# Performance work log

Hardware: AMD Instinct MI355X
Metric: run time of the kernel (lower is better)

## Reference

```python
import jax, jax.numpy as jnp
import numpy as np

ORDER = 3        # spline degree k
NUM_KNOTS = 64   # knots param from __init__


def setup_inputs() -> dict:
    key = jax.random.key(0)
    kx, kc = jax.random.split(key)
    # elementwise activation input; values outside [0,1] exercise scipy-style extrapolation
    x = jax.random.normal(kx, (4, 4096, 4096), dtype=jnp.float32)
    # nn.Parameter(torch.randn(num_knots + order))
    coefficients = jax.random.normal(kc, (NUM_KNOTS + ORDER,), dtype=jnp.float32)
    return {"x": x, "coefficients": coefficients}


def reference(x, coefficients):
    p = ORDER
    # knots = np.linspace(0, 1, num_knots + 2*order)
    t = jnp.linspace(0.0, 1.0, NUM_KNOTS + 2 * p).astype(x.dtype)
    n = t.shape[0] - p - 1  # number of basis functions scipy actually uses
    c = coefficients[:n]    # scipy ignores trailing extra coefficients

    # knot-span index; clipping to [p, n-1] reproduces extrapolate=True
    i = jnp.clip(jnp.searchsorted(t, x, side="right") - 1, p, n - 1)

    # de Boor recursion, vectorized over all elements of x
    d = [c[i - p + j] for j in range(p + 1)]  # each has shape of x
    for r in range(1, p + 1):
        for j in range(p, r - 1, -1):
            left = t[i + j - p]
            right = t[i + 1 + j - r]
            alpha = (x - left) / (right - left)
            d[j] = (1.0 - alpha) * d[j - 1] + alpha * d[j]
    return d[p]
```

## Files before the change

### kernel.cpp

```cpp
#include <hip/hip_runtime.h>

#define NCOEF 66
#define H     (1.0f/69.0f)

__device__ __forceinline__ float eval_spline(float xx, const float* __restrict__ c) {
    int i = (int)(xx * 69.0f);
    i = i < 3 ? 3 : (i > 65 ? 65 : i);

    float ti = (float)i * H;
    float u  = xx - ti;
    float u1 = u + H;
    float u2 = u + 2.0f * H;

    float d0 = c[i - 3];
    float d1 = c[i - 2];
    float d2 = c[i - 1];
    float d3 = c[i];

    float a;
    a = u  * 23.0f; d3 = (1.0f - a) * d2 + a * d3;
    a = u1 * 23.0f; d2 = (1.0f - a) * d1 + a * d2;
    a = u2 * 23.0f; d1 = (1.0f - a) * d0 + a * d1;
    a = u  * 34.5f; d3 = (1.0f - a) * d2 + a * d3;
    a = u1 * 34.5f; d2 = (1.0f - a) * d1 + a * d2;
    a = u  * 69.0f; d3 = (1.0f - a) * d2 + a * d3;
    return d3;
}

__global__ __launch_bounds__(256) void spline_kernel(
    const float* __restrict__ x, const float* __restrict__ coef,
    float* __restrict__ out, int n)
{
    __shared__ float c[NCOEF];
    if (threadIdx.x < NCOEF) c[threadIdx.x] = coef[threadIdx.x];
    __syncthreads();

    const int n4     = n >> 2;
    const int stride = gridDim.x * blockDim.x;
    int idx = blockIdx.x * blockDim.x + threadIdx.x;

    for (; idx < n4; idx += stride) {
        float4 xv = reinterpret_cast<const float4*>(x)[idx];
        float4 ov;
        ov.x = eval_spline(xv.x, c);
        ov.y = eval_spline(xv.y, c);
        ov.z = eval_spline(xv.z, c);
        ov.w = eval_spline(xv.w, c);
        reinterpret_cast<float4*>(out)[idx] = ov;
    }

    int tail = (n4 << 2) + (blockIdx.x * blockDim.x + threadIdx.x);
    if (tail < n && (blockIdx.x * blockDim.x + threadIdx.x) < (n & 3)) {
        out[tail] = eval_spline(x[tail], c);
    }
}

extern "C" void kernel_launch(void* const* d_in, const int* in_sizes, int n_in,
                              void* d_out, int out_size, void* d_ws, size_t ws_size,
                              hipStream_t stream) {
    const float* x    = (const float*)d_in[0];
    const float* coef = (const float*)d_in[1];
    float* out        = (float*)d_out;
    int n = in_sizes[0];

    int n4 = n >> 2;
    int threads = 256;
    int blocks = 4096;
    int max_blocks = (n4 + threads - 1) / threads;
    if (blocks > max_blocks) blocks = max_blocks;
    if (blocks < 1) blocks = 1;

    spline_kernel<<<blocks, threads, 0, stream>>>(x, coef, out, n);
}
```

Before: 433.4 us.

## Precompute per-span cubic polynomial coefficients and evaluate via Horner

Each block now converts the 66 B-spline coefficients into per-span cubic polynomial coefficients (uniform-knot B-spline matrix) stored as float4 in shared memory. Per element, the de Boor recursion becomes a single float4 LDS lookup and three FMAs. The grid size also grows to 8192 blocks. The main cost targeted is ALU and LDS work per element; since the kernel streams 256MB in and out it is likely memory bound, so any gain may be small. Rounding differs slightly from the recursion.

```diff
diff --git a/kernel.cpp b/kernel.cpp
--- a/kernel.cpp
+++ b/kernel.cpp
@@ -1,57 +1,56 @@
 #include <hip/hip_runtime.h>
 
 #define NCOEF 66
-#define H     (1.0f/69.0f)
 
-__device__ __forceinline__ float eval_spline(float xx, const float* __restrict__ c) {
-    int i = (int)(xx * 69.0f);
-    i = i < 3 ? 3 : (i > 65 ? 65 : i);
-
-    float ti = (float)i * H;
-    float u  = xx - ti;
-    float u1 = u + H;
-    float u2 = u + 2.0f * H;
-
-    float d0 = c[i - 3];
-    float d1 = c[i - 2];
-    float d2 = c[i - 1];
-    float d3 = c[i];
-
-    float a;
-    a = u  * 23.0f; d3 = (1.0f - a) * d2 + a * d3;
-    a = u1 * 23.0f; d2 = (1.0f - a) * d1 + a * d2;
-    a = u2 * 23.0f; d1 = (1.0f - a) * d0 + a * d1;
-    a = u  * 34.5f; d3 = (1.0f - a) * d2 + a * d3;
-    a = u1 * 34.5f; d2 = (1.0f - a) * d1 + a * d2;
-    a = u  * 69.0f; d3 = (1.0f - a) * d2 + a * d3;
-    return d3;
-}
 
 __global__ __launch_bounds__(256) void spline_kernel(
     const float* __restrict__ x, const float* __restrict__ coef,
     float* __restrict__ out, int n)
 {
-    __shared__ float c[NCOEF];
-    if (threadIdx.x < NCOEF) c[threadIdx.x] = coef[threadIdx.x];
+    __shared__ float  sc[NCOEF];
+    __shared__ float4 tab[NCOEF];
+
+    const int t = threadIdx.x;
+    if (t < NCOEF) sc[t] = coef[t];
+    __syncthreads();
+    if (t >= 3 && t < NCOEF) {
+        float c0 = sc[t - 3], c1 = sc[t - 2], c2 = sc[t - 1], c3 = sc[t];
+        const float k6 = 1.0f / 6.0f;
+        float a0 = (c0 + 4.0f * c1 + c2) * k6;
+        float a1 = (c2 - c0) * 0.5f;
+        float a2 = (c0 - 2.0f * c1 + c2) * 0.5f;
+        float a3 = (c3 - c0 + 3.0f * (c1 - c2)) * k6;
+        tab[t] = make_float4(a0, a1, a2, a3);
+    }
     __syncthreads();
 
     const int n4     = n >> 2;
     const int stride = gridDim.x * blockDim.x;
-    int idx = blockIdx.x * blockDim.x + threadIdx.x;
+    const int gid    = blockIdx.x * blockDim.x + threadIdx.x;
 
-    for (; idx < n4; idx += stride) {
+    for (int idx = gid; idx < n4; idx += stride) {
         float4 xv = reinterpret_cast<const float4*>(x)[idx];
         float4 ov;
-        ov.x = eval_spline(xv.x, c);
-        ov.y = eval_spline(xv.y, c);
-        ov.z = eval_spline(xv.z, c);
-        ov.w = eval_spline(xv.w, c);
+        #pragma unroll
+        for (int e = 0; e < 4; ++e) {
+            float xx = (&xv.x)[e];
+            float xs = xx * 69.0f;
+            int   i  = (int)xs;
+            i = i < 3 ? 3 : (i > 65 ? 65 : i);
+            float s  = xs - (float)i;
+            float4 a = tab[i];
+            (&ov.x)[e] = fmaf(fmaf(fmaf(a.w, s, a.z), s, a.y), s, a.x);
+        }
         reinterpret_cast<float4*>(out)[idx] = ov;
     }
 
-    int tail = (n4 << 2) + (blockIdx.x * blockDim.x + threadIdx.x);
-    if (tail < n && (blockIdx.x * blockDim.x + threadIdx.x) < (n & 3)) {
-        out[tail] = eval_spline(x[tail], c);
+    for (int k = (n4 << 2) + gid; k < n; k += stride) {
+        float xs = x[k] * 69.0f;
+        int   i  = (int)xs;
+        i = i < 3 ? 3 : (i > 65 ? 65 : i);
+        float s  = xs - (float)i;
+        float4 a = tab[i];
+        out[k] = fmaf(fmaf(fmaf(a.w, s, a.z), s, a.y), s, a.x);
     }
 }
 
@@ -63,12 +62,11 @@
     float* out        = (float*)d_out;
     int n = in_sizes[0];
 
-    int n4 = n >> 2;
     int threads = 256;
-    int blocks = 4096;
-    int max_blocks = (n4 + threads - 1) / threads;
+    int blocks  = 8192;
+    int max_blocks = ((n >> 2) + threads - 1) / threads;
+    if (max_blocks < 1) max_blocks = 1;
     if (blocks > max_blocks) blocks = max_blocks;
-    if (blocks < 1) blocks = 1;
 
     spline_kernel<<<blocks, threads, 0, stream>>>(x, coef, out, n);
 }
```

Measured after the change: 431.8 us. No clear change (-0.4%).
